# Performance work log

Measured on AMD Instinct MI355X. Metric: run time of the kernel, lower is better.

## Reference

```python
import jax, jax.numpy as jnp
import numpy as np

EPS = 1e-8

def _batch_gather(table, idx):
    # table: (B, M, F), idx: (B, K) -> (B, K, F)
    return jnp.take_along_axis(table, idx[:, :, None], axis=1)

def setup_inputs() -> dict:
    key = jax.random.key(0)
    ks = jax.random.split(key, 8)
    B, N, E, K, F = 8, 4096, 16384, 16, 128
    initial_node_embed = jax.random.normal(ks[0], (B, N, F), dtype=jnp.float32)
    edges = jax.random.randint(ks[1], (B, E, 3), 0, N, dtype=jnp.int64)
    node_edges = jax.random.randint(ks[2], (B, N, K), 0, E, dtype=jnp.int64)
    node_edge_mask = jax.random.randint(ks[3], (B, N, K), 0, 2, dtype=jnp.int32)
    s = 1.0 / np.sqrt(F)
    W1 = jax.random.normal(ks[4], (F, F), dtype=jnp.float32) * s
    b1 = jnp.zeros((F,), dtype=jnp.float32)
    W2 = jax.random.normal(ks[5], (F, F), dtype=jnp.float32) * s
    b2 = jnp.zeros((F,), dtype=jnp.float32)
    return {"initial_node_embed": initial_node_embed, "edges": edges,
            "node_edges": node_edges, "node_edge_mask": node_edge_mask,
            "W1": W1, "b1": b1, "W2": W2, "b2": b2}

def reference(initial_node_embed, edges, node_edges, node_edge_mask, W1, b1, W2, b2):
    B, N, F = initial_node_embed.shape
    K = node_edges.shape[2]
    sender_idx = edges[:, :, 0]                      # (B, E)
    mask_f = node_edge_mask.astype(jnp.float32)      # (B, N, K)
    num_neighbors = jnp.sum(mask_f, 2, keepdims=True) + EPS  # (B, N, 1)
    flat_ne = node_edges.reshape(B, -1)              # (B, N*K)

    def mp(node_emb, W, b):
        sender = _batch_gather(node_emb, sender_idx)             # (B, E, F)
        edge_emb = jnp.tanh(sender @ W.T + b)                    # (B, E, F)
        nbr = _batch_gather(edge_emb, flat_ne).reshape(B, N, K, F)
        nbr = nbr * mask_f[:, :, :, None]
        return jnp.sum(nbr, 2) / num_neighbors                   # avg agg

    x0 = initial_node_embed
    x1 = mp(x0, W1, b1)
    x2 = mp(x1, W2, b2)
    return jnp.concatenate([x0, x1, x2], axis=2)     # (B, N, 3F)
```

## Files before the change

kernel.cpp:

```cpp
#include <hip/hip_runtime.h>
#include <hip/hip_bf16.h>

typedef __attribute__((ext_vector_type(8))) short short8;
typedef __attribute__((ext_vector_type(4))) float f32x4;
typedef __attribute__((ext_vector_type(2))) float f32x2;

#define B_ 8
#define N_ 4096
#define E_ 16384
#define K_ 16
#define F_ 128

#if defined(__has_builtin)
#  if __has_builtin(__builtin_amdgcn_cvt_pk_f32_fp8) && __has_builtin(__builtin_amdgcn_cvt_pk_fp8_f32)
#    define HW_FP8 1
#  endif
#endif

__device__ __forceinline__ unsigned short f2bf(float f) {
    union { float f; unsigned int u; } c; c.f = f;
    unsigned int u = c.u;
    unsigned int r = (u + 0x7fffu + ((u >> 16) & 1u)) >> 16;
    return (unsigned short)r;
}
__device__ __forceinline__ float fast_tanh(float x) {
    float e = __expf(2.0f * x);
    return 1.0f - 2.0f / (e + 1.0f);
}

__device__ __forceinline__ unsigned int f2fp8_manual(float v) {
    unsigned int u = __float_as_uint(v * 0x1p-120f);
    unsigned int r = (u & 0x7fffffffu) + 0x7ffffu + ((u >> 20) & 1u);
    return ((r >> 20) & 0x7fu) | ((u >> 24) & 0x80u);
}
__device__ __forceinline__ unsigned int pack_fp8x4(float t0, float t1, float t2, float t3) {
#ifdef HW_FP8
    int wd = 0;
    wd = __builtin_amdgcn_cvt_pk_fp8_f32(t0, t1, wd, false);
    wd = __builtin_amdgcn_cvt_pk_fp8_f32(t2, t3, wd, true);
    return (unsigned int)wd;
#else
    return f2fp8_manual(t0) | (f2fp8_manual(t1) << 8) |
           (f2fp8_manual(t2) << 16) | (f2fp8_manual(t3) << 24);
#endif
}
#ifndef HW_FP8
#define DECM(bb) __int_as_float((int)((((bb) & 0x80u) << 24) | (((bb) & 0x7fu) << 20)))
#endif

__device__ __forceinline__ int detect64(const int* raw) {
    int o = 0;
    #pragma unroll
    for (int i = 1; i < 128; i += 2) o |= raw[i];
    return (o == 0) ? 1 : 0;
}

__global__ void wprep(const float* __restrict__ W1, const float* __restrict__ W2,
                      const int* __restrict__ edges_raw, const int* __restrict__ ne_raw,
                      unsigned short* __restrict__ wf, int* __restrict__ flags) {
    int blk = blockIdx.x, tid = threadIdx.x;
    if (blk == 16) {
        if (tid == 0) {
            flags[0] = detect64(edges_raw);
            flags[1] = detect64(ne_raw);
        }
        return;
    }
    int gtid = blk * 256 + tid;
    int wsel = gtid >> 11;
    int q = gtid & 2047;
    int lane = q & 63;
    int gq = q >> 6;
    int nt = gq >> 2, g = gq & 3;
    const float* W = wsel ? W2 : W1;
    int j = nt * 16 + (lane & 15);
    int kbase = g * 32 + 8 * (lane >> 4);
    unsigned short* d = wf + wsel * 16384 + q * 8;
    #pragma unroll
    for (int t = 0; t < 8; ++t) d[t] = f2bf(W[j * 128 + kbase + t]);
}

template <int SRC, int DO_AUX>
__global__ void __launch_bounds__(256) node_kernel(
    const void* __restrict__ xsrc, const int* __restrict__ edges_raw,
    const int* __restrict__ ne_raw, const int* __restrict__ mask,
    const int* __restrict__ flags, const unsigned short* __restrict__ wf,
    const float* __restrict__ bias, unsigned char* __restrict__ y,
    float* __restrict__ out, int* __restrict__ sid2) {
    __shared__ short xt[64 * F_];
    int tid = threadIdx.x;
    int swz = (blockIdx.x & 7) * 64 + (blockIdx.x >> 3);
    int b = swz >> 6;
    int r0 = (swz & 63) * 64;
    if (DO_AUX) {
        int s64e = flags[0], s64n = flags[1];
        int base = swz * 1024;
        #pragma unroll
        for (int t = 0; t < 4; ++t) {
            int i = base + t * 256 + tid;
            int bb = i >> 16;
            int eid = s64n ? ne_raw[2 * (long long)i] : ne_raw[i];
            long long ei = (long long)(bb * E_ + eid);
            int s = s64e ? edges_raw[6 * ei] : edges_raw[3 * ei];
            sid2[i] = mask[i] ? s : -1;
        }
    }
    #pragma unroll
    for (int c = 0; c < 4; ++c) {
        int ci = tid + 256 * c;
        int row = ci >> 4, ch = ci & 15;
        int pch = ch ^ (row & 15);
        long long gnode = (long long)(b * N_ + r0 + row);
        if (SRC == 1) {
            const float* src = (const float*)xsrc + gnode * F_ + ch * 8;
            float4 v0 = *(const float4*)src;
            float4 v1 = *(const float4*)(src + 4);
            ushort4 h0, h1;
            h0.x = f2bf(v0.x); h0.y = f2bf(v0.y); h0.z = f2bf(v0.z); h0.w = f2bf(v0.w);
            h1.x = f2bf(v1.x); h1.y = f2bf(v1.y); h1.z = f2bf(v1.z); h1.w = f2bf(v1.w);
            *(ushort4*)&xt[row * F_ + pch * 8] = h0;
            *(ushort4*)&xt[row * F_ + pch * 8 + 4] = h1;
            if (DO_AUX) {
                float* od = out + gnode * 384 + ch * 8;
                *(float4*)od = v0;
                *(float4*)(od + 4) = v1;
            }
        } else {
            const unsigned char* src = (const unsigned char*)xsrc + gnode * F_ + ch * 8;
            uint2 v = *(const uint2*)src;
            short8 h;
#ifdef HW_FP8
            f32x2 c0 = __builtin_amdgcn_cvt_pk_f32_fp8(v.x, false);
            f32x2 c1 = __builtin_amdgcn_cvt_pk_f32_fp8(v.x, true);
            f32x2 c2 = __builtin_amdgcn_cvt_pk_f32_fp8(v.y, false);
            f32x2 c3 = __builtin_amdgcn_cvt_pk_f32_fp8(v.y, true);
            h[0] = (short)f2bf(c0.x); h[1] = (short)f2bf(c0.y);
            h[2] = (short)f2bf(c1.x); h[3] = (short)f2bf(c1.y);
            h[4] = (short)f2bf(c2.x); h[5] = (short)f2bf(c2.y);
            h[6] = (short)f2bf(c3.x); h[7] = (short)f2bf(c3.y);
#else
            h[0] = (short)f2bf(0x1p120f * DECM(v.x));
            h[1] = (short)f2bf(0x1p120f * DECM(v.x >> 8));
            h[2] = (short)f2bf(0x1p120f * DECM(v.x >> 16));
            h[3] = (short)f2bf(0x1p120f * DECM(v.x >> 24));
            h[4] = (short)f2bf(0x1p120f * DECM(v.y));
            h[5] = (short)f2bf(0x1p120f * DECM(v.y >> 8));
            h[6] = (short)f2bf(0x1p120f * DECM(v.y >> 16));
            h[7] = (short)f2bf(0x1p120f * DECM(v.y >> 24));
#endif
            *(short8*)&xt[row * F_ + pch * 8] = h;
        }
    }
    __syncthreads();
    int w = tid >> 6, lane = tid & 63;
    int rr = w * 16 + (lane & 15);
    short8 bfr[4];
    #pragma unroll
    for (int g = 0; g < 4; ++g) {
        int pch = (g * 4 + (lane >> 4)) ^ (rr & 15);
        bfr[g] = *(const short8*)&xt[rr * F_ + pch * 8];
    }
    int jq = (lane >> 4) * 4;
    long long ybyte = ((long long)(b * N_ + r0 + w * 16 + (lane & 15))) * F_;
    #pragma unroll
    for (int nt = 0; nt < 8; ++nt) {
        f32x4 acc = (f32x4){0.f, 0.f, 0.f, 0.f};
        #pragma unroll
        for (int g = 0; g < 4; ++g) {
            short8 afr = *(const short8*)(wf + ((nt * 4 + g) * 64 + lane) * 8);
            acc = __builtin_amdgcn_mfma_f32_16x16x32_bf16(afr, bfr[g], acc, 0, 0, 0);
        }
        float4 bv = *(const float4*)(bias + nt * 16 + jq);
        float t0 = fast_tanh(acc[0] + bv.x);
        float t1 = fast_tanh(acc[1] + bv.y);
        float t2 = fast_tanh(acc[2] + bv.z);
        float t3 = fast_tanh(acc[3] + bv.w);
        *(unsigned int*)(y + ybyte + nt * 16 + jq) = pack_fp8x4(t0, t1, t2, t3);
    }
}

__global__ void __launch_bounds__(256) agg_kernel(
    const unsigned char* __restrict__ y, const int* __restrict__ sid2,
    float* __restrict__ out, unsigned char* __restrict__ xf8, int col_off) {
    int tid = threadIdx.x;
    int swz = (blockIdx.x & 7) * 256 + (blockIdx.x >> 3);
    int nodeblk = swz * 16;
    int wid = tid >> 6, lane = tid & 63;
    int qt = lane >> 4, s16 = lane & 15;
    int node = nodeblk + wid * 4 + qt;
    int b = node >> 12;
    const int4* ip = (const int4*)(sid2 + node * K_);
    int4 i0 = ip[0], i1 = ip[1], i2 = ip[2], i3 = ip[3];
    float cnt = (float)((i0.x >= 0) + (i0.y >= 0) + (i0.z >= 0) + (i0.w >= 0) +
                        (i1.x >= 0) + (i1.y >= 0) + (i1.z >= 0) + (i1.w >= 0) +
                        (i2.x >= 0) + (i2.y >= 0) + (i2.z >= 0) + (i2.w >= 0) +
                        (i3.x >= 0) + (i3.y >= 0) + (i3.z >= 0) + (i3.w >= 0));
    const unsigned char* ybase = y + (long long)b * (N_ * F_) + s16 * 8;
    float a0 = 0.f, a1 = 0.f, a2 = 0.f, a3 = 0.f;
    float a4 = 0.f, a5 = 0.f, a6 = 0.f, a7 = 0.f;
#ifdef HW_FP8
    #define PROC(pk) { \
        float m = ((pk) >= 0) ? 1.0f : 0.0f; \
        int nid = (pk) < 0 ? 0 : (pk); \
        uint2 v = *(const uint2*)(ybase + (long long)nid * F_); \
        f32x2 c0 = __builtin_amdgcn_cvt_pk_f32_fp8(v.x, false); \
        f32x2 c1 = __builtin_amdgcn_cvt_pk_f32_fp8(v.x, true); \
        f32x2 c2 = __builtin_amdgcn_cvt_pk_f32_fp8(v.y, false); \
        f32x2 c3 = __builtin_amdgcn_cvt_pk_f32_fp8(v.y, true); \
        a0 += m * c0.x; a1 += m * c0.y; a2 += m * c1.x; a3 += m * c1.y; \
        a4 += m * c2.x; a5 += m * c2.y; a6 += m * c3.x; a7 += m * c3.y; }
#else
    #define PROC(pk) { \
        float ms = ((pk) >= 0) ? 0x1p120f : 0.0f; \
        int nid = (pk) < 0 ? 0 : (pk); \
        uint2 v = *(const uint2*)(ybase + (long long)nid * F_); \
        a0 += ms * DECM(v.x); a1 += ms * DECM(v.x >> 8); \
        a2 += ms * DECM(v.x >> 16); a3 += ms * DECM(v.x >> 24); \
        a4 += ms * DECM(v.y); a5 += ms * DECM(v.y >> 8); \
        a6 += ms * DECM(v.y >> 16); a7 += ms * DECM(v.y >> 24); }
#endif
    PROC(i0.x) PROC(i0.y) PROC(i0.z) PROC(i0.w)
    PROC(i1.x) PROC(i1.y) PROC(i1.z) PROC(i1.w)
    PROC(i2.x) PROC(i2.y) PROC(i2.z) PROC(i2.w)
    PROC(i3.x) PROC(i3.y) PROC(i3.z) PROC(i3.w)
    #undef PROC
    float inv = 1.0f / (cnt + 1e-8f);
    a0 *= inv; a1 *= inv; a2 *= inv; a3 *= inv;
    a4 *= inv; a5 *= inv; a6 *= inv; a7 *= inv;
    float* po = out + (long long)node * 384 + col_off + s16 * 8;
    *(f32x4*)po = (f32x4){a0, a1, a2, a3};
    *(f32x4*)(po + 4) = (f32x4){a4, a5, a6, a7};
    if (xf8) {
        uint2 p;
        p.x = pack_fp8x4(a0, a1, a2, a3);
        p.y = pack_fp8x4(a4, a5, a6, a7);
        *(uint2*)(xf8 + (long long)node * F_ + s16 * 8) = p;
    }
}

extern "C" void kernel_launch(void* const* d_in, const int* in_sizes, int n_in,
                              void* d_out, int out_size, void* d_ws, size_t ws_size,
                              hipStream_t stream) {
    const float* x0        = (const float*)d_in[0];
    const int*   edges_raw = (const int*)d_in[1];
    const int*   ne_raw    = (const int*)d_in[2];
    const int*   mask      = (const int*)d_in[3];
    const float* W1        = (const float*)d_in[4];
    const float* b1        = (const float*)d_in[5];
    const float* W2        = (const float*)d_in[6];
    const float* b2        = (const float*)d_in[7];
    float* out = (float*)d_out;
    char* ws = (char*)d_ws;

    unsigned char*  ybuf = (unsigned char*)ws;
    unsigned char*  x1f8 = (unsigned char*)(ws + 4194304);
    unsigned short* wf   = (unsigned short*)(ws + 8388608);
    int* flags           = (int*)(ws + 8454144);
    int* sid2            = (int*)(ws + 8519680);

    wprep<<<17, 256, 0, stream>>>(W1, W2, edges_raw, ne_raw, wf, flags);
    node_kernel<1, 1><<<512, 256, 0, stream>>>(x0, edges_raw, ne_raw, mask,
                                               flags, wf, b1, ybuf, out, sid2);
    agg_kernel<<<2048, 256, 0, stream>>>(ybuf, sid2, out, x1f8, 128);
    node_kernel<2, 0><<<512, 256, 0, stream>>>(x1f8, edges_raw, ne_raw, mask,
                                               flags, wf + 16384, b2, ybuf, nullptr, nullptr);
    agg_kernel<<<2048, 256, 0, stream>>>(ybuf, sid2, out, nullptr, 256);
}
```

Before: 48.59 us.

## Fuse layer-1 aggregation with layer-2 node transform into one kernel

Merges the first aggregation and the second matmul+tanh stage into a single kernel. Aggregated rows go straight into shared memory as bf16 instead of being written to global memory as fp8 and read back. This drops one launch and a round trip through global memory, and it removes the fp8 quantisation of x1. The cost is fewer blocks (512 instead of 2048) doing the gather-heavy aggregation, so there is less parallelism for hiding latency. A separate y2 buffer is used to avoid a read/write hazard.

Result: faster. 46.88 us, median of 2 (-3.5%).

```diff
diff --git a/kernel.cpp b/kernel.cpp
--- a/kernel.cpp
+++ b/kernel.cpp
@@ -80,9 +80,8 @@
     for (int t = 0; t < 8; ++t) d[t] = f2bf(W[j * 128 + kbase + t]);
 }
 
-template <int SRC, int DO_AUX>
 __global__ void __launch_bounds__(256) node_kernel(
-    const void* __restrict__ xsrc, const int* __restrict__ edges_raw,
+    const float* __restrict__ xsrc, const int* __restrict__ edges_raw,
     const int* __restrict__ ne_raw, const int* __restrict__ mask,
     const int* __restrict__ flags, const unsigned short* __restrict__ wf,
     const float* __restrict__ bias, unsigned char* __restrict__ y,
@@ -92,7 +91,7 @@
     int swz = (blockIdx.x & 7) * 64 + (blockIdx.x >> 3);
     int b = swz >> 6;
     int r0 = (swz & 63) * 64;
-    if (DO_AUX) {
+    {
         int s64e = flags[0], s64n = flags[1];
         int base = swz * 1024;
         #pragma unroll
@@ -111,45 +110,17 @@
         int row = ci >> 4, ch = ci & 15;
         int pch = ch ^ (row & 15);
         long long gnode = (long long)(b * N_ + r0 + row);
-        if (SRC == 1) {
-            const float* src = (const float*)xsrc + gnode * F_ + ch * 8;
-            float4 v0 = *(const float4*)src;
-            float4 v1 = *(const float4*)(src + 4);
-            ushort4 h0, h1;
-            h0.x = f2bf(v0.x); h0.y = f2bf(v0.y); h0.z = f2bf(v0.z); h0.w = f2bf(v0.w);
-            h1.x = f2bf(v1.x); h1.y = f2bf(v1.y); h1.z = f2bf(v1.z); h1.w = f2bf(v1.w);
-            *(ushort4*)&xt[row * F_ + pch * 8] = h0;
-            *(ushort4*)&xt[row * F_ + pch * 8 + 4] = h1;
-            if (DO_AUX) {
-                float* od = out + gnode * 384 + ch * 8;
-                *(float4*)od = v0;
-                *(float4*)(od + 4) = v1;
-            }
-        } else {
-            const unsigned char* src = (const unsigned char*)xsrc + gnode * F_ + ch * 8;
-            uint2 v = *(const uint2*)src;
-            short8 h;
-#ifdef HW_FP8
-            f32x2 c0 = __builtin_amdgcn_cvt_pk_f32_fp8(v.x, false);
-            f32x2 c1 = __builtin_amdgcn_cvt_pk_f32_fp8(v.x, true);
-            f32x2 c2 = __builtin_amdgcn_cvt_pk_f32_fp8(v.y, false);
-            f32x2 c3 = __builtin_amdgcn_cvt_pk_f32_fp8(v.y, true);
-            h[0] = (short)f2bf(c0.x); h[1] = (short)f2bf(c0.y);
-            h[2] = (short)f2bf(c1.x); h[3] = (short)f2bf(c1.y);
-            h[4] = (short)f2bf(c2.x); h[5] = (short)f2bf(c2.y);
-            h[6] = (short)f2bf(c3.x); h[7] = (short)f2bf(c3.y);
-#else
-            h[0] = (short)f2bf(0x1p120f * DECM(v.x));
-            h[1] = (short)f2bf(0x1p120f * DECM(v.x >> 8));
-            h[2] = (short)f2bf(0x1p120f * DECM(v.x >> 16));
-            h[3] = (short)f2bf(0x1p120f * DECM(v.x >> 24));
-            h[4] = (short)f2bf(0x1p120f * DECM(v.y));
-            h[5] = (short)f2bf(0x1p120f * DECM(v.y >> 8));
-            h[6] = (short)f2bf(0x1p120f * DECM(v.y >> 16));
-            h[7] = (short)f2bf(0x1p120f * DECM(v.y >> 24));
-#endif
-            *(short8*)&xt[row * F_ + pch * 8] = h;
-        }
+        const float* src = xsrc + gnode * F_ + ch * 8;
+        float4 v0 = *(const float4*)src;
+        float4 v1 = *(const float4*)(src + 4);
+        ushort4 h0, h1;
+        h0.x = f2bf(v0.x); h0.y = f2bf(v0.y); h0.z = f2bf(v0.z); h0.w = f2bf(v0.w);
+        h1.x = f2bf(v1.x); h1.y = f2bf(v1.y); h1.z = f2bf(v1.z); h1.w = f2bf(v1.w);
+        *(ushort4*)&xt[row * F_ + pch * 8] = h0;
+        *(ushort4*)&xt[row * F_ + pch * 8 + 4] = h1;
+        float* od = out + gnode * 384 + ch * 8;
+        *(float4*)od = v0;
+        *(float4*)(od + 4) = v1;
     }
     __syncthreads();
     int w = tid >> 6, lane = tid & 63;
@@ -179,9 +150,100 @@
     }
 }
 
+__global__ void __launch_bounds__(256) aggnode_kernel(
+    const unsigned char* __restrict__ y1, const int* __restrict__ sid2,
+    const unsigned short* __restrict__ wf2, const float* __restrict__ bias,
+    float* __restrict__ out, unsigned char* __restrict__ y2) {
+    __shared__ short xt[64 * F_];
+    int tid = threadIdx.x;
+    int swz = (blockIdx.x & 7) * 64 + (blockIdx.x >> 3);
+    int b = swz >> 6;
+    int r0 = (swz & 63) * 64;
+    int wid = tid >> 6, lane = tid & 63;
+    int qt = lane >> 4, s16 = lane & 15;
+    const unsigned char* ybase = y1 + (long long)b * (N_ * F_) + s16 * 8;
+    #pragma unroll
+    for (int t = 0; t < 4; ++t) {
+        int row = wid * 16 + qt * 4 + t;
+        long long gnode = (long long)(b * N_ + r0 + row);
+        const int4* ip = (const int4*)(sid2 + gnode * K_);
+        int4 i0 = ip[0], i1 = ip[1], i2 = ip[2], i3 = ip[3];
+        float cnt = (float)((i0.x >= 0) + (i0.y >= 0) + (i0.z >= 0) + (i0.w >= 0) +
+                            (i1.x >= 0) + (i1.y >= 0) + (i1.z >= 0) + (i1.w >= 0) +
+                            (i2.x >= 0) + (i2.y >= 0) + (i2.z >= 0) + (i2.w >= 0) +
+                            (i3.x >= 0) + (i3.y >= 0) + (i3.z >= 0) + (i3.w >= 0));
+        float a0 = 0.f, a1 = 0.f, a2 = 0.f, a3 = 0.f;
+        float a4 = 0.f, a5 = 0.f, a6 = 0.f, a7 = 0.f;
+#ifdef HW_FP8
+        #define PROC(pk) { \
+            float m = ((pk) >= 0) ? 1.0f : 0.0f; \
+            int nid = (pk) < 0 ? 0 : (pk); \
+            uint2 v = *(const uint2*)(ybase + (long long)nid * F_); \
+            f32x2 c0 = __builtin_amdgcn_cvt_pk_f32_fp8(v.x, false); \
+            f32x2 c1 = __builtin_amdgcn_cvt_pk_f32_fp8(v.x, true); \
+            f32x2 c2 = __builtin_amdgcn_cvt_pk_f32_fp8(v.y, false); \
+            f32x2 c3 = __builtin_amdgcn_cvt_pk_f32_fp8(v.y, true); \
+            a0 += m * c0.x; a1 += m * c0.y; a2 += m * c1.x; a3 += m * c1.y; \
+            a4 += m * c2.x; a5 += m * c2.y; a6 += m * c3.x; a7 += m * c3.y; }
+#else
+        #define PROC(pk) { \
+            float ms = ((pk) >= 0) ? 0x1p120f : 0.0f; \
+            int nid = (pk) < 0 ? 0 : (pk); \
+            uint2 v = *(const uint2*)(ybase + (long long)nid * F_); \
+            a0 += ms * DECM(v.x); a1 += ms * DECM(v.x >> 8); \
+            a2 += ms * DECM(v.x >> 16); a3 += ms * DECM(v.x >> 24); \
+            a4 += ms * DECM(v.y); a5 += ms * DECM(v.y >> 8); \
+            a6 += ms * DECM(v.y >> 16); a7 += ms * DECM(v.y >> 24); }
+#endif
+        PROC(i0.x) PROC(i0.y) PROC(i0.z) PROC(i0.w)
+        PROC(i1.x) PROC(i1.y) PROC(i1.z) PROC(i1.w)
+        PROC(i2.x) PROC(i2.y) PROC(i2.z) PROC(i2.w)
+        PROC(i3.x) PROC(i3.y) PROC(i3.z) PROC(i3.w)
+        #undef PROC
+        float inv = 1.0f / (cnt + 1e-8f);
+        a0 *= inv; a1 *= inv; a2 *= inv; a3 *= inv;
+        a4 *= inv; a5 *= inv; a6 *= inv; a7 *= inv;
+        float* po = out + gnode * 384 + 128 + s16 * 8;
+        *(f32x4*)po = (f32x4){a0, a1, a2, a3};
+        *(f32x4*)(po + 4) = (f32x4){a4, a5, a6, a7};
+        int pch = s16 ^ (row & 15);
+        short8 h;
+        h[0] = (short)f2bf(a0); h[1] = (short)f2bf(a1);
+        h[2] = (short)f2bf(a2); h[3] = (short)f2bf(a3);
+        h[4] = (short)f2bf(a4); h[5] = (short)f2bf(a5);
+        h[6] = (short)f2bf(a6); h[7] = (short)f2bf(a7);
+        *(short8*)&xt[row * F_ + pch * 8] = h;
+    }
+    __syncthreads();
+    int rr = wid * 16 + (lane & 15);
+    short8 bfr[4];
+    #pragma unroll
+    for (int g = 0; g < 4; ++g) {
+        int pch = (g * 4 + (lane >> 4)) ^ (rr & 15);
+        bfr[g] = *(const short8*)&xt[rr * F_ + pch * 8];
+    }
+    int jq = (lane >> 4) * 4;
+    long long ybyte = ((long long)(b * N_ + r0 + wid * 16 + (lane & 15))) * F_;
+    #pragma unroll
+    for (int nt = 0; nt < 8; ++nt) {
+        f32x4 acc = (f32x4){0.f, 0.f, 0.f, 0.f};
+        #pragma unroll
+        for (int g = 0; g < 4; ++g) {
+            short8 afr = *(const short8*)(wf2 + ((nt * 4 + g) * 64 + lane) * 8);
+            acc = __builtin_amdgcn_mfma_f32_16x16x32_bf16(afr, bfr[g], acc, 0, 0, 0);
+        }
+        float4 bv = *(const float4*)(bias + nt * 16 + jq);
+        float t0 = fast_tanh(acc[0] + bv.x);
+        float t1 = fast_tanh(acc[1] + bv.y);
+        float t2 = fast_tanh(acc[2] + bv.z);
+        float t3 = fast_tanh(acc[3] + bv.w);
+        *(unsigned int*)(y2 + ybyte + nt * 16 + jq) = pack_fp8x4(t0, t1, t2, t3);
+    }
+}
+
 __global__ void __launch_bounds__(256) agg_kernel(
     const unsigned char* __restrict__ y, const int* __restrict__ sid2,
-    float* __restrict__ out, unsigned char* __restrict__ xf8, int col_off) {
+    float* __restrict__ out, int col_off) {
     int tid = threadIdx.x;
     int swz = (blockIdx.x & 7) * 256 + (blockIdx.x >> 3);
     int nodeblk = swz * 16;
@@ -230,12 +292,6 @@
     float* po = out + (long long)node * 384 + col_off + s16 * 8;
     *(f32x4*)po = (f32x4){a0, a1, a2, a3};
     *(f32x4*)(po + 4) = (f32x4){a4, a5, a6, a7};
-    if (xf8) {
-        uint2 p;
-        p.x = pack_fp8x4(a0, a1, a2, a3);
-        p.y = pack_fp8x4(a4, a5, a6, a7);
-        *(uint2*)(xf8 + (long long)node * F_ + s16 * 8) = p;
-    }
 }
 
 extern "C" void kernel_launch(void* const* d_in, const int* in_sizes, int n_in,
@@ -252,17 +308,15 @@
     float* out = (float*)d_out;
     char* ws = (char*)d_ws;
 
-    unsigned char*  ybuf = (unsigned char*)ws;
-    unsigned char*  x1f8 = (unsigned char*)(ws + 4194304);
+    unsigned char*  y1   = (unsigned char*)ws;
+    unsigned char*  y2   = (unsigned char*)(ws + 4194304);
     unsigned short* wf   = (unsigned short*)(ws + 8388608);
     int* flags           = (int*)(ws + 8454144);
     int* sid2            = (int*)(ws + 8519680);
 
     wprep<<<17, 256, 0, stream>>>(W1, W2, edges_raw, ne_raw, wf, flags);
-    node_kernel<1, 1><<<512, 256, 0, stream>>>(x0, edges_raw, ne_raw, mask,
-                                               flags, wf, b1, ybuf, out, sid2);
-    agg_kernel<<<2048, 256, 0, stream>>>(ybuf, sid2, out, x1f8, 128);
-    node_kernel<2, 0><<<512, 256, 0, stream>>>(x1f8, edges_raw, ne_raw, mask,
-                                               flags, wf + 16384, b2, ybuf, nullptr, nullptr);
-    agg_kernel<<<2048, 256, 0, stream>>>(ybuf, sid2, out, nullptr, 256);
-}
+    node_kernel<<<512, 256, 0, stream>>>(x0, edges_raw, ne_raw, mask,
+                                         flags, wf, b1, y1, out, sid2);
+    aggnode_kernel<<<512, 256, 0, stream>>>(y1, sid2, wf + 16384, b2, out, y2);
+    agg_kernel<<<2048, 256, 0, stream>>>(y2, sid2, out, 256);
+}
```
